# Kernel optimization log

Hardware: AMD Instinct MI355X
Metric: run time of the kernel (lower is better)

The kernel has to match this reference:

```python
import jax, jax.numpy as jnp
import numpy as np

N_NODES = 100000
N_EDGES = 1200000
D = 64          # hidden_feat_dim == out_feat_dim
D_CELL = 16     # cell_feat_dim
HID = 256       # MLP hidden width (from MLP(..., 256, ...))
N_TGT = 50000


def setup_inputs() -> dict:
    key = jax.random.key(0)
    ks = jax.random.split(key, 13)
    inv = lambda d: 1.0 / np.sqrt(d)
    return {
        "h": jax.random.normal(ks[0], (N_NODES, D), jnp.float32),
        "cell_feat": jax.random.normal(ks[1], (N_NODES, D_CELL), jnp.float32),
        "src": jax.random.randint(ks[2], (N_EDGES,), 0, N_NODES, jnp.int32),
        "dst": jax.random.randint(ks[3], (N_EDGES,), 0, N_NODES, jnp.int32),
        "targets": jax.random.randint(ks[4], (N_TGT,), 0, N_NODES, jnp.int32),
        "Wn1": jax.random.normal(ks[5], (D, HID), jnp.float32) * inv(D),
        "bn1": jnp.zeros((HID,), jnp.float32),
        "Wn2": jax.random.normal(ks[6], (HID, D), jnp.float32) * inv(HID),
        "bn2": jnp.zeros((D,), jnp.float32),
        "Ws1": jax.random.normal(ks[7], (D_CELL, HID), jnp.float32) * inv(D_CELL),
        "bs1": jnp.zeros((HID,), jnp.float32),
        "Ws2": jax.random.normal(ks[8], (HID, D), jnp.float32) * inv(HID),
        "bs2": jnp.zeros((D,), jnp.float32),
    }


def _mlp2(x, W1, b1, W2, b2):
    # MLP(d_in, 256, d_out) with LeakyReLU(negative_slope=0) == ReLU
    return jax.nn.relu(x @ W1 + b1) @ W2 + b2


def reference(h, cell_feat, src, dst, targets,
              Wn1, bn1, Wn2, bn2, Ws1, bs1, Ws2, bs2):
    # PathConv forward, even level_id > 0, flag_attn=False:
    #   pull(copy_src('h','m'), cell_msg_reduce, apply_cell_func) on 'cell' edges
    N = h.shape[0]
    m = h[src]  # gather edge messages [E, D]
    # cell_msg_reduce: per-dst, per-channel softmax over incoming messages
    mmax = jax.ops.segment_max(m, dst, num_segments=N)          # [N, D]
    mmax = jnp.where(jnp.isfinite(mmax), mmax, 0.0)             # isolated nodes
    e = jnp.exp(m - mmax[dst])                                  # [E, D]
    den = jax.ops.segment_sum(e, dst, num_segments=N)           # [N, D]
    num = jax.ops.segment_sum(e * m, dst, num_segments=N)       # sum(msg*softmax)
    h_neigh1 = num / jnp.where(den == 0.0, 1.0, den)            # [N, D]
    # apply_cell_func: fc_cell_self(cell_feat) + fc_cell_neigh(h_neigh1)
    h_new = _mlp2(cell_feat, Ws1, bs1, Ws2, bs2) + _mlp2(h_neigh1, Wn1, bn1, Wn2, bn2)
    h_new = jax.nn.relu(h_new)  # self.activation
    return h_new[targets]
```

## Files before the change

kernel.cpp:

```cpp
#include <hip/hip_runtime.h>

#define NN 100000
#define NE 1200000
#define DD 64
#define DC 16
#define DH 256
#define NT 50000
#define MAXDEG 64

typedef __attribute__((ext_vector_type(8))) short bf16x8;
typedef __attribute__((ext_vector_type(4))) float f32x4;

__device__ __forceinline__ unsigned short f2bf(float x) {
    unsigned int u = __float_as_uint(x);
    return (unsigned short)((u + 0x7FFFu + ((u >> 16) & 1u)) >> 16);
}
__device__ __forceinline__ float bf2f(unsigned short b) {
    return __uint_as_float(((unsigned int)b) << 16);
}

__device__ __forceinline__ void split8t(const float* p, bf16x8& hi, bf16x8& lo) {
    f32x4 a = *reinterpret_cast<const f32x4*>(p);
    f32x4 b = *reinterpret_cast<const f32x4*>(p + 4);
    #pragma unroll
    for (int j = 0; j < 4; ++j) {
        unsigned short h = (unsigned short)(__float_as_uint(a[j]) >> 16);
        hi[j] = (short)h;
        lo[j] = (short)(__float_as_uint(a[j] - bf2f(h)) >> 16);
    }
    #pragma unroll
    for (int j = 0; j < 4; ++j) {
        unsigned short h = (unsigned short)(__float_as_uint(b[j]) >> 16);
        hi[4 + j] = (short)h;
        lo[4 + j] = (short)(__float_as_uint(b[j] - bf2f(h)) >> 16);
    }
}

#define N_W1NT 16384
#define N_W1SP 8192
#define N_W2C  32768
#define N_PACK (N_W1NT + N_W1SP + N_W2C)
#define N_PREP NN

__global__ __launch_bounds__(256) void prep_k(
    const float* __restrict__ Wn1, const float* __restrict__ Ws1,
    const float* __restrict__ Wn2, const float* __restrict__ Ws2,
    unsigned short* __restrict__ W1nT, unsigned short* __restrict__ W1sP,
    unsigned short* __restrict__ W2c,
    int* __restrict__ ifl, int* __restrict__ deg)
{
    int tid = blockIdx.x * 256 + threadIdx.x;
    if (tid < NN) ifl[tid] = -1;
    if (tid < NT + 16) deg[tid] = 0;
    if (tid >= N_PACK) return;
    float v; unsigned short* ph; int idx;
    if (tid < N_W1NT) {
        idx = tid;
        int j = idx & 7, l = (idx >> 3) & 63, rest = idx >> 9;
        int ks = rest & 1, c = rest >> 1;
        int feat = ks * 32 + ((l >> 4) << 3) + j, hid = (c << 4) + (l & 15);
        v = Wn1[(size_t)feat * DH + hid];
        ph = W1nT;
    } else if (tid < N_W1NT + N_W1SP) {
        idx = tid - N_W1NT;
        int j = idx & 7, l = (idx >> 3) & 63, c = idx >> 9;
        int k = ((l >> 4) << 3) + j, hid = (c << 4) + (l & 15);
        v = Ws1[(size_t)(k & 15) * DH + hid];
        ph = W1sP;
    } else {
        idx = tid - N_W1NT - N_W1SP;
        int j = idx & 7, l = (idx >> 3) & 63, rest = idx >> 9;
        int u = rest & 3, c = rest >> 2;
        int row = (c << 4) + ((l >> 4) << 2) + (j & 3), col = (u << 4) + (l & 15);
        v = (j < 4) ? Wn2[(size_t)row * DD + col] : Ws2[(size_t)row * DD + col];
        ph = W2c;
    }
    ph[idx] = f2bf(v);
}

__global__ __launch_bounds__(256) void mark_wl_k(
    const int* __restrict__ tg, int* __restrict__ ifl, int* __restrict__ cnt)
{
    int i = blockIdx.x * 256 + threadIdx.x;
    int lane = threadIdx.x & 63;
    bool claim = false;
    int t = 0;
    if (i < NT) {
        t = tg[i];
        claim = (atomicCAS(&ifl[t], -1, -2) == -1);
    }
    unsigned long long mask = __ballot(claim);
    if (mask == 0ull) return;
    int nclaim = __popcll(mask);
    int leader = __ffsll((unsigned long long)mask) - 1;
    int base = 0;
    if (lane == leader) base = atomicAdd(cnt, nclaim);
    base = __shfl(base, leader);
    if (claim) {
        int rank = __popcll(mask & ((1ull << lane) - 1ull));
        ifl[t] = base + rank;
    }
}

#define NE4 (NE / 4)
#define N_SCAT (NE4 > NT ? NE4 : NT)

__global__ __launch_bounds__(256) void scatter_tgw_k(
    const int4* __restrict__ src4, const int4* __restrict__ dst4,
    const int* __restrict__ ifl, const int* __restrict__ tg,
    int* __restrict__ tgw, int* __restrict__ deg, int* __restrict__ csr)
{
    int tid = blockIdx.x * 256 + threadIdx.x;
    if (tid < NE4) {
        int4 d = dst4[tid];
        int4 s = src4[tid];
        int w;
        w = ifl[d.x]; if (w >= 0) { int sl = atomicAdd(&deg[w], 1); if (sl < MAXDEG) csr[w * MAXDEG + sl] = s.x; }
        w = ifl[d.y]; if (w >= 0) { int sl = atomicAdd(&deg[w], 1); if (sl < MAXDEG) csr[w * MAXDEG + sl] = s.y; }
        w = ifl[d.z]; if (w >= 0) { int sl = atomicAdd(&deg[w], 1); if (sl < MAXDEG) csr[w * MAXDEG + sl] = s.z; }
        w = ifl[d.w]; if (w >= 0) { int sl = atomicAdd(&deg[w], 1); if (sl < MAXDEG) csr[w * MAXDEG + sl] = s.w; }
    }
    if (tid < NT) tgw[tid] = ifl[tg[tid]];
}

__global__ __launch_bounds__(256) void reduce_k(
    const float* __restrict__ h, const int* __restrict__ csr,
    const int* __restrict__ deg, const int* __restrict__ cnt,
    float* __restrict__ hn_c)
{
    int gw = (blockIdx.x * 256 + threadIdx.x) >> 6;
    int lane = threadIdx.x & 63;
    if (gw >= cnt[0]) return;
    int g = min(deg[gw], MAXDEG);
    int sid = csr[gw * MAXDEG + lane];
    if (lane >= g) sid = 0;
    const int e4 = lane >> 4, c4 = lane & 15;

    f32x4 accd = {0.f, 0.f, 0.f, 0.f}, accn = {0.f, 0.f, 0.f, 0.f};
    for (int base = 0; base < g; base += 16) {
        f32x4 m[4];
        bool  val[4];
        #pragma unroll
        for (int bb = 0; bb < 4; ++bb) {
            int idx = base + bb * 4 + e4;
            val[bb] = (idx < g);
            if (base + bb * 4 < g) {
                int s = __shfl(sid, idx);
                m[bb] = *reinterpret_cast<const f32x4*>(
                            h + (size_t)s * DD + c4 * 4);
            } else {
                m[bb] = f32x4{0.f, 0.f, 0.f, 0.f};
                val[bb] = false;
            }
        }
        #pragma unroll
        for (int bb = 0; bb < 4; ++bb) {
            #pragma unroll
            for (int r = 0; r < 4; ++r) {
                float ex = __expf(m[bb][r]);
                ex = val[bb] ? ex : 0.f;
                accd[r] += ex;
                accn[r] = fmaf(ex, m[bb][r], accn[r]);
            }
        }
    }
    #pragma unroll
    for (int r = 0; r < 4; ++r) {
        accd[r] += __shfl_xor(accd[r], 16);
        accn[r] += __shfl_xor(accn[r], 16);
        accd[r] += __shfl_xor(accd[r], 32);
        accn[r] += __shfl_xor(accn[r], 32);
    }
    if (lane < 16) {
        f32x4 o;
        #pragma unroll
        for (int r = 0; r < 4; ++r)
            o[r] = (accd[r] == 0.f) ? 0.f : accn[r] / accd[r];
        *reinterpret_cast<f32x4*>(hn_c + (size_t)gw * DD + c4 * 4) = o;
    }
}

#define NT32 ((NT + 31) / 32)

__global__ __launch_bounds__(256, 6) void mfma_mlp_k(
    const float* __restrict__ hn_c, const int* __restrict__ tgw,
    const float* __restrict__ cellf, const int* __restrict__ tg,
    const unsigned short* __restrict__ W1nT, const unsigned short* __restrict__ W1sP,
    const unsigned short* __restrict__ W2c,
    const float* __restrict__ bn1, const float* __restrict__ bs1,
    const float* __restrict__ bn2, const float* __restrict__ bs2,
    float* __restrict__ out)
{
    __shared__ float shbuf[32 * 84];
    float (*X)[84]      = reinterpret_cast<float(*)[84]>(shbuf);
    float (*Ys)[16][68] = reinterpret_cast<float(*)[16][68]>(shbuf);

    const int tid = threadIdx.x;
    const int wv = tid >> 6, ln = tid & 63;
    const int l16 = ln & 15, kb = (ln >> 4) << 3;
    const int sg = wv >> 1;
    const int hf = wv & 1;
    const int rbase = blockIdx.x * 32;

    {
        int r = tid >> 3, seg = tid & 7;
        int row = rbase + r; if (row >= NT) row = NT - 1;
        int w = tgw[row];
        const float* hp = hn_c + (size_t)w * DD + seg * 8;
        *reinterpret_cast<f32x4*>(&X[r][seg * 8])     = *reinterpret_cast<const f32x4*>(hp);
        *reinterpret_cast<f32x4*>(&X[r][seg * 8 + 4]) = *reinterpret_cast<const f32x4*>(hp + 4);
        if (seg < 4) {
            int t2 = tg[row];
            *reinterpret_cast<f32x4*>(&X[r][64 + seg * 4]) =
                *reinterpret_cast<const f32x4*>(cellf + (size_t)t2 * DC + seg * 4);
        }
    }
    __syncthreads();

    const float* xrow = X[sg * 16 + l16];
    bf16x8 xh[2], xl[2];
    #pragma unroll
    for (int ks = 0; ks < 2; ++ks)
        split8t(&xrow[ks * 32 + kb], xh[ks], xl[ks]);
    bf16x8 sx;
    {
        const float* cp = &xrow[64 + (kb & 8)];
        f32x4 a = *reinterpret_cast<const f32x4*>(cp);
        f32x4 b = *reinterpret_cast<const f32x4*>(cp + 4);
        #pragma unroll
        for (int j = 0; j < 4; ++j) {
            unsigned short hh = (unsigned short)(__float_as_uint(a[j]) >> 16);
            sx[j] = (ln < 32) ? (short)hh
                              : (short)(__float_as_uint(a[j] - bf2f(hh)) >> 16);
        }
        #pragma unroll
        for (int j = 0; j < 4; ++j) {
            unsigned short hh = (unsigned short)(__float_as_uint(b[j]) >> 16);
            sx[4 + j] = (ln < 32) ? (short)hh
                                  : (short)(__float_as_uint(b[j] - bf2f(hh)) >> 16);
        }
    }
    __syncthreads();

    f32x4 accY[4];
    #pragma unroll
    for (int u = 0; u < 4; ++u) accY[u] = f32x4{0.f, 0.f, 0.f, 0.f};

    #pragma unroll
    for (int c8 = 0; c8 < 8; ++c8) {
        const int cg = hf * 8 + c8;
        f32x4 a1 = *reinterpret_cast<const f32x4*>(bn1 + cg * 16 + ((ln >> 4) << 2));
        #pragma unroll
        for (int ks = 0; ks < 2; ++ks) {
            bf16x8 wh = *reinterpret_cast<const bf16x8*>(W1nT + (((cg * 2 + ks) * 64 + ln) << 3));
            a1 = __builtin_amdgcn_mfma_f32_16x16x32_bf16(wh, xh[ks], a1, 0, 0, 0);
            a1 = __builtin_amdgcn_mfma_f32_16x16x32_bf16(wh, xl[ks], a1, 0, 0, 0);
        }
        f32x4 a1s = *reinterpret_cast<const f32x4*>(bs1 + cg * 16 + ((ln >> 4) << 2));
        {
            bf16x8 whs = *reinterpret_cast<const bf16x8*>(W1sP + ((cg * 64 + ln) << 3));
            a1s = __builtin_amdgcn_mfma_f32_16x16x32_bf16(whs, sx, a1s, 0, 0, 0);
        }
        bf16x8 ph, pl;
        #pragma unroll
        for (int r = 0; r < 4; ++r) {
            float d = fmaxf(a1[r], 0.f);
            unsigned short hh = (unsigned short)(__float_as_uint(d) >> 16);
            ph[r] = (short)hh;
            pl[r] = (short)(__float_as_uint(d - bf2f(hh)) >> 16);
            float ds = fmaxf(a1s[r], 0.f);
            unsigned short hs = (unsigned short)(__float_as_uint(ds) >> 16);
            ph[4 + r] = (short)hs;
            pl[4 + r] = (short)(__float_as_uint(ds - bf2f(hs)) >> 16);
        }
        #pragma unroll
        for (int u = 0; u < 4; ++u) {
            bf16x8 w2 = *reinterpret_cast<const bf16x8*>(W2c + (((cg * 4 + u) * 64 + ln) << 3));
            accY[u] = __builtin_amdgcn_mfma_f32_16x16x32_bf16(ph, w2, accY[u], 0, 0, 0);
            accY[u] = __builtin_amdgcn_mfma_f32_16x16x32_bf16(pl, w2, accY[u], 0, 0, 0);
        }
    }

    if (hf == 1) {
        #pragma unroll
        for (int u = 0; u < 4; ++u)
            #pragma unroll
            for (int r = 0; r < 4; ++r)
                Ys[sg][(ln >> 4) * 4 + r][u * 16 + l16] = accY[u][r];
    }
    __syncthreads();
    if (hf == 0) {
        const int s4 = (ln >> 4) << 2;
        #pragma unroll
        for (int u = 0; u < 4; ++u) {
            float b2 = bn2[u * 16 + l16] + bs2[u * 16 + l16];
            #pragma unroll
            for (int r = 0; r < 4; ++r) {
                int rowg = rbase + sg * 16 + s4 + r;
                if (rowg < NT)
                    out[(size_t)rowg * DD + u * 16 + l16] =
                        fmaxf(accY[u][r] + Ys[sg][s4 + r][u * 16 + l16] + b2, 0.f);
            }
        }
    }
}

extern "C" void kernel_launch(void* const* d_in, const int* in_sizes, int n_in,
                              void* d_out, int out_size, void* d_ws, size_t ws_size,
                              hipStream_t stream)
{
    const float* h     = (const float*)d_in[0];
    const float* cellf = (const float*)d_in[1];
    const int*   src   = (const int*)d_in[2];
    const int*   dst   = (const int*)d_in[3];
    const int*   tg    = (const int*)d_in[4];
    const float* Wn1   = (const float*)d_in[5];
    const float* bn1   = (const float*)d_in[6];
    const float* Wn2   = (const float*)d_in[7];
    const float* bn2   = (const float*)d_in[8];
    const float* Ws1   = (const float*)d_in[9];
    const float* bs1   = (const float*)d_in[10];
    const float* Ws2   = (const float*)d_in[11];
    const float* bs2   = (const float*)d_in[12];
    float* out = (float*)d_out;

    int*   ifl  = (int*)d_ws;
    int*   deg  = ifl + NN;
    int*   cnt  = deg + NT;
    int*   tgw  = cnt + 16;
    int*   csr  = tgw + NT;
    float* hn_c = (float*)(csr + (size_t)NT * MAXDEG);
    size_t woff = ((size_t)((char*)(hn_c + (size_t)NT * DD) - (char*)d_ws) + 63)
                  & ~(size_t)63;
    unsigned short* W1nT = (unsigned short*)((char*)d_ws + woff);
    unsigned short* W1sP = W1nT + N_W1NT;
    unsigned short* W2c  = W1sP + N_W1SP;

    prep_k<<<(N_PREP + 255) / 256, 256, 0, stream>>>(
        Wn1, Ws1, Wn2, Ws2, W1nT, W1sP, W2c, ifl, deg);

    mark_wl_k<<<(NT + 255) / 256, 256, 0, stream>>>(tg, ifl, cnt);

    scatter_tgw_k<<<(N_SCAT + 255) / 256, 256, 0, stream>>>(
        (const int4*)src, (const int4*)dst, ifl, tg, tgw, deg, csr);

    reduce_k<<<NT / 4, 256, 0, stream>>>(h, csr, deg, cnt, hn_c);

    mfma_mlp_k<<<NT32, 256, 0, stream>>>(hn_c, tgw, cellf, tg,
        W1nT, W1sP, W2c, bn1, bs1, bn2, bs2, out);
}
```

Baseline: 90.77 us.

## Split MLP hidden dim across four waves per 16-row tile; load CSR ids directly

The MLP kernel now handles 16 target rows per block instead of 32. Each of the four waves takes a quarter of the 256 hidden channels, and three waves' partial outputs are summed through shared memory by wave 0. This doubles the block count and shortens each wave's serial MFMA chain, at the cost of more shared-memory reduction traffic and more redundant weight loads per output row. Separately, the reduce kernel drops the per-wave CSR load plus shuffle broadcast and reads neighbour ids from global memory at each step.

```diff
diff --git a/kernel.cpp b/kernel.cpp
--- a/kernel.cpp
+++ b/kernel.cpp
@@ -132,9 +132,8 @@
     int lane = threadIdx.x & 63;
     if (gw >= cnt[0]) return;
     int g = min(deg[gw], MAXDEG);
-    int sid = csr[gw * MAXDEG + lane];
-    if (lane >= g) sid = 0;
     const int e4 = lane >> 4, c4 = lane & 15;
+    const int* crow = csr + gw * MAXDEG;
 
     f32x4 accd = {0.f, 0.f, 0.f, 0.f}, accn = {0.f, 0.f, 0.f, 0.f};
     for (int base = 0; base < g; base += 16) {
@@ -145,9 +144,9 @@
             int idx = base + bb * 4 + e4;
             val[bb] = (idx < g);
             if (base + bb * 4 < g) {
-                int s = __shfl(sid, idx);
+                int id = crow[min(idx, g - 1)];
                 m[bb] = *reinterpret_cast<const f32x4*>(
-                            h + (size_t)s * DD + c4 * 4);
+                            h + (size_t)id * DD + c4 * 4);
             } else {
                 m[bb] = f32x4{0.f, 0.f, 0.f, 0.f};
                 val[bb] = false;
@@ -180,7 +179,7 @@
     }
 }
 
-#define NT32 ((NT + 31) / 32)
+#define NT16 ((NT + 15) / 16)
 
 __global__ __launch_bounds__(256, 6) void mfma_mlp_k(
     const float* __restrict__ hn_c, const int* __restrict__ tgw,
@@ -191,24 +190,21 @@
     const float* __restrict__ bn2, const float* __restrict__ bs2,
     float* __restrict__ out)
 {
-    __shared__ float shbuf[32 * 84];
+    __shared__ float shbuf[3 * 16 * 68];
     float (*X)[84]      = reinterpret_cast<float(*)[84]>(shbuf);
     float (*Ys)[16][68] = reinterpret_cast<float(*)[16][68]>(shbuf);
 
     const int tid = threadIdx.x;
     const int wv = tid >> 6, ln = tid & 63;
     const int l16 = ln & 15, kb = (ln >> 4) << 3;
-    const int sg = wv >> 1;
-    const int hf = wv & 1;
-    const int rbase = blockIdx.x * 32;
+    const int rbase = blockIdx.x * 16;
 
     {
-        int r = tid >> 3, seg = tid & 7;
+        int r = tid >> 4, seg = tid & 15;
         int row = rbase + r; if (row >= NT) row = NT - 1;
         int w = tgw[row];
-        const float* hp = hn_c + (size_t)w * DD + seg * 8;
-        *reinterpret_cast<f32x4*>(&X[r][seg * 8])     = *reinterpret_cast<const f32x4*>(hp);
-        *reinterpret_cast<f32x4*>(&X[r][seg * 8 + 4]) = *reinterpret_cast<const f32x4*>(hp + 4);
+        *reinterpret_cast<f32x4*>(&X[r][seg * 4]) =
+            *reinterpret_cast<const f32x4*>(hn_c + (size_t)w * DD + seg * 4);
         if (seg < 4) {
             int t2 = tg[row];
             *reinterpret_cast<f32x4*>(&X[r][64 + seg * 4]) =
@@ -217,7 +213,7 @@
     }
     __syncthreads();
 
-    const float* xrow = X[sg * 16 + l16];
+    const float* xrow = X[l16];
     bf16x8 xh[2], xl[2];
     #pragma unroll
     for (int ks = 0; ks < 2; ++ks)
@@ -247,8 +243,8 @@
     for (int u = 0; u < 4; ++u) accY[u] = f32x4{0.f, 0.f, 0.f, 0.f};
 
     #pragma unroll
-    for (int c8 = 0; c8 < 8; ++c8) {
-        const int cg = hf * 8 + c8;
+    for (int c = 0; c < 4; ++c) {
+        const int cg = wv * 4 + c;
         f32x4 a1 = *reinterpret_cast<const f32x4*>(bn1 + cg * 16 + ((ln >> 4) << 2));
         #pragma unroll
         for (int ks = 0; ks < 2; ++ks) {
@@ -281,25 +277,29 @@
         }
     }
 
-    if (hf == 1) {
+    if (wv > 0) {
         #pragma unroll
         for (int u = 0; u < 4; ++u)
             #pragma unroll
             for (int r = 0; r < 4; ++r)
-                Ys[sg][(ln >> 4) * 4 + r][u * 16 + l16] = accY[u][r];
+                Ys[wv - 1][(ln >> 4) * 4 + r][u * 16 + l16] = accY[u][r];
     }
     __syncthreads();
-    if (hf == 0) {
+    if (wv == 0) {
         const int s4 = (ln >> 4) << 2;
         #pragma unroll
         for (int u = 0; u < 4; ++u) {
             float b2 = bn2[u * 16 + l16] + bs2[u * 16 + l16];
             #pragma unroll
             for (int r = 0; r < 4; ++r) {
-                int rowg = rbase + sg * 16 + s4 + r;
-                if (rowg < NT)
-                    out[(size_t)rowg * DD + u * 16 + l16] =
-                        fmaxf(accY[u][r] + Ys[sg][s4 + r][u * 16 + l16] + b2, 0.f);
+                int rowg = rbase + s4 + r;
+                if (rowg < NT) {
+                    float sum = accY[u][r] + b2
+                              + Ys[0][s4 + r][u * 16 + l16]
+                              + Ys[1][s4 + r][u * 16 + l16]
+                              + Ys[2][s4 + r][u * 16 + l16];
+                    out[(size_t)rowg * DD + u * 16 + l16] = fmaxf(sum, 0.f);
+                }
             }
         }
     }
@@ -346,6 +346,6 @@
 
     reduce_k<<<NT / 4, 256, 0, stream>>>(h, csr, deg, cnt, hn_c);
 
-    mfma_mlp_k<<<NT32, 256, 0, stream>>>(hn_c, tgw, cellf, tg,
+    mfma_mlp_k<<<NT16, 256, 0, stream>>>(hn_c, tgw, cellf, tg,
         W1nT, W1sP, W2c, bn1, bs1, bn2, bs2, out);
 }
```

Result: slower. 92.62 us (+2.0%).
